# Optimization experiments

Hardware: AMD Instinct MI355X
Metric: run time of the kernel (lower is better)

## Reference

```python
import jax, jax.numpy as jnp
import numpy as np

H = 2048
V = 50257
M = 64

def setup_inputs() -> dict:
    key = jax.random.key(0)
    ks = jax.random.split(key, 14)
    s = 0.02  # weight init scale for numerical sanity
    return {
        "input_tok": jax.random.randint(ks[0], (1,), 0, V),
        "hidden": jax.random.normal(ks[1], (1, 1, H), jnp.float32),
        "encoder_outputs": jax.random.normal(ks[2], (M, H), jnp.float32),
        "emb": jax.random.normal(ks[3], (V, H), jnp.float32) * s,
        "attn_w": jax.random.normal(ks[4], (M, 2 * H), jnp.float32) * s,
        "attn_b": jax.random.normal(ks[5], (M,), jnp.float32) * s,
        "comb_w": jax.random.normal(ks[6], (H, 2 * H), jnp.float32) * s,
        "comb_b": jax.random.normal(ks[7], (H,), jnp.float32) * s,
        "w_ih": jax.random.normal(ks[8], (3 * H, H), jnp.float32) * s,
        "w_hh": jax.random.normal(ks[9], (3 * H, H), jnp.float32) * s,
        "b_ih": jax.random.normal(ks[10], (3 * H,), jnp.float32) * s,
        "b_hh": jax.random.normal(ks[11], (3 * H,), jnp.float32) * s,
        "out_w": jax.random.normal(ks[12], (V, H), jnp.float32) * s,
        "out_b": jax.random.normal(ks[13], (V,), jnp.float32) * s,
    }

def reference(input_tok, hidden, encoder_outputs, emb, attn_w, attn_b,
              comb_w, comb_b, w_ih, w_hh, b_ih, b_hh, out_w, out_b):
    # embedded: [1, H] (dropout is eval-mode identity)
    embedded = emb[input_tok].reshape(1, H)
    h0 = hidden[0]  # [1, H]
    # Bahdanau-style attention over encoder outputs
    attn_weights = jax.nn.softmax(
        jnp.concatenate([embedded, h0], axis=1) @ attn_w.T + attn_b, axis=1)  # [1, M]
    attn_applied = attn_weights @ encoder_outputs  # [1, H]
    # combine + relu
    x = jnp.concatenate([embedded, attn_applied], axis=1) @ comb_w.T + comb_b
    x = jax.nn.relu(x)  # [1, H] -> GRU input
    # single GRU cell step, PyTorch gate order (r, z, n)
    gi = x @ w_ih.T + b_ih   # [1, 3H]
    gh = h0 @ w_hh.T + b_hh  # [1, 3H]
    i_r, i_z, i_n = jnp.split(gi, 3, axis=1)
    h_r, h_z, h_n = jnp.split(gh, 3, axis=1)
    r = jax.nn.sigmoid(i_r + h_r)
    z = jax.nn.sigmoid(i_z + h_z)
    n = jnp.tanh(i_n + r * h_n)
    h_new = (1.0 - z) * n + z * h0  # [1, H]
    # output projection + log-softmax over vocab
    log_probs = jax.nn.log_softmax(h_new @ out_w.T + out_b, axis=1)  # [1, V]
    return (log_probs, h_new[None], attn_weights)
```

## Files before the change

kernel.cpp:

```cpp
#include <hip/hip_runtime.h>
#include <math.h>

#define H 2048
#define V 50257
#define M 64
#define NEG_BIG (-1.0e30f)

#define NB5 6283
#define NB6 197

typedef float f4 __attribute__((ext_vector_type(4)));

__device__ inline f4 ntload(const f4* p) { return __builtin_nontemporal_load(p); }
__device__ inline float dot4(f4 a, f4 b) { return a.x*b.x + a.y*b.y + a.z*b.z + a.w*b.w; }

__device__ inline float wred_sum(float v) {
#pragma unroll
    for (int o = 32; o >= 1; o >>= 1) v += __shfl_down(v, o);
    return v;
}

__global__ void k_scores_gh1(const int* __restrict__ tok, const float* __restrict__ hidden,
                             const float* __restrict__ emb, const float* __restrict__ attn_w,
                             const float* __restrict__ attn_b, const float* __restrict__ w_hh,
                             const float* __restrict__ b_hh, float* __restrict__ scores,
                             float* __restrict__ gh) {
    const int t = threadIdx.x, lane = t & 63, wid = t >> 6;
    if (blockIdx.x < 64) {
        const int m = blockIdx.x;
        const float* erow = emb + (size_t)tok[0] * H;
        const f4* w4 = (const f4*)(attn_w + (size_t)m * 2 * H);
        float acc = 0.f;
        for (int i = t; i < 1024; i += 256) {
            f4 w = ntload(w4 + i);
            int k = i * 4;
            f4 c = (k < H) ? *(const f4*)(erow + k) : *(const f4*)(hidden + (k - H));
            acc += dot4(w, c);
        }
        __shared__ float sred[4];
        float s = wred_sum(acc);
        if (lane == 0) sred[wid] = s;
        __syncthreads();
        if (t == 0) scores[m] = sred[0] + sred[1] + sred[2] + sred[3] + attn_b[m];
    } else {
        const int j = (blockIdx.x - 64) * 4 + wid;
        const f4* w4 = (const f4*)(w_hh + (size_t)j * H);
        const f4* h4 = (const f4*)hidden;
        float acc = 0.f;
#pragma unroll
        for (int it = 0; it < 8; ++it) {
            int i = it * 64 + lane;
            acc += dot4(ntload(w4 + i), h4[i]);
        }
        acc = wred_sum(acc);
        if (lane == 0) gh[j] = acc + b_hh[j];
    }
}

__global__ void k_sm_aa_gh2(const float* __restrict__ scores, const float* __restrict__ enc,
                            const float* __restrict__ hidden, const float* __restrict__ w_hh,
                            const float* __restrict__ b_hh, float* __restrict__ aw_out,
                            float* __restrict__ attn_applied, float* __restrict__ gh) {
    const int t = threadIdx.x, lane = t & 63, wid = t >> 6;
    if (blockIdx.x < 8) {
        __shared__ float w[M];
        if (t < 64) {
            float s = scores[t];
            float mx = s;
#pragma unroll
            for (int o = 32; o >= 1; o >>= 1) mx = fmaxf(mx, __shfl_xor(mx, o));
            float e = expf(s - mx);
            float sum = e;
#pragma unroll
            for (int o = 32; o >= 1; o >>= 1) sum += __shfl_xor(sum, o);
            float aw = e / sum;
            w[t] = aw;
            if (blockIdx.x == 0) aw_out[t] = aw;
        }
        __syncthreads();
        int h = blockIdx.x * 256 + t;
        float acc = 0.f;
#pragma unroll 8
        for (int m = 0; m < M; ++m) acc += w[m] * enc[(size_t)m * H + h];
        attn_applied[h] = acc;
    } else {
        const int j = 3072 + (blockIdx.x - 8) * 4 + wid;
        const f4* w4 = (const f4*)(w_hh + (size_t)j * H);
        const f4* h4 = (const f4*)hidden;
        float acc = 0.f;
#pragma unroll
        for (int it = 0; it < 8; ++it) {
            int i = it * 64 + lane;
            acc += dot4(ntload(w4 + i), h4[i]);
        }
        acc = wred_sum(acc);
        if (lane == 0) gh[j] = acc + b_hh[j];
    }
}

__global__ void k_combine(const int* __restrict__ tok, const float* __restrict__ emb,
                          const float* __restrict__ comb_w, const float* __restrict__ comb_b,
                          const float* __restrict__ aa, float* __restrict__ x_out) {
    int r = (blockIdx.x * blockDim.x + threadIdx.x) >> 6;
    int lane = threadIdx.x & 63;
    const float* erow = emb + (size_t)tok[0] * H;
    const f4* w4 = (const f4*)(comb_w + (size_t)r * 2 * H);
    float acc = 0.f;
#pragma unroll
    for (int it = 0; it < 16; ++it) {
        int i = it * 64 + lane;
        f4 w = ntload(w4 + i);
        int k = i * 4;
        f4 c = (k < H) ? *(const f4*)(erow + k) : *(const f4*)(aa + (k - H));
        acc += dot4(w, c);
    }
    acc = wred_sum(acc);
    if (lane == 0) x_out[r] = fmaxf(acc + comb_b[r], 0.f);
}

__global__ void k_gates(const float* __restrict__ hidden, const float* __restrict__ w_ih,
                        const float* __restrict__ b_ih, const float* __restrict__ x,
                        const float* __restrict__ gh, float* __restrict__ h_out) {
    int j = (blockIdx.x * blockDim.x + threadIdx.x) >> 6;
    int lane = threadIdx.x & 63;
    const f4* x4 = (const f4*)x;
    const f4* wr = (const f4*)(w_ih + (size_t)j * H);
    const f4* wz = (const f4*)(w_ih + (size_t)(H + j) * H);
    const f4* wn = (const f4*)(w_ih + (size_t)(2 * H + j) * H);
    float ar = 0.f, az = 0.f, an = 0.f;
#pragma unroll
    for (int it = 0; it < 8; ++it) {
        int i = it * 64 + lane;
        f4 xv = x4[i];
        ar += dot4(ntload(wr + i), xv);
        az += dot4(ntload(wz + i), xv);
        an += dot4(ntload(wn + i), xv);
    }
    ar = wred_sum(ar); az = wred_sum(az); an = wred_sum(an);
    if (lane == 0) {
        float r = 1.f / (1.f + expf(-(ar + b_ih[j] + gh[j])));
        float z = 1.f / (1.f + expf(-(az + b_ih[H + j] + gh[H + j])));
        float n = tanhf(an + b_ih[2 * H + j] + r * gh[2 * H + j]);
        h_out[j] = (1.f - z) * n + z * hidden[j];
    }
}

__global__ void k_logits(const float* __restrict__ out_w, const float* __restrict__ out_b,
                         const float* __restrict__ hnew, float* __restrict__ logits,
                         float2* __restrict__ part) {
    const int t = threadIdx.x, lane = t & 63, wid = t >> 6;
    const int base = (blockIdx.x * 4 + wid) * 2;
    const int row0 = base, row1 = base + 1;
    const bool v0 = row0 < V, v1 = row1 < V;
    const f4* w0 = (const f4*)(out_w + (size_t)(v0 ? row0 : 0) * H);
    const f4* w1 = (const f4*)(out_w + (size_t)(v1 ? row1 : 0) * H);
    const f4* h4 = (const f4*)hnew;
    float a0 = 0.f, a1 = 0.f;
#pragma unroll
    for (int it = 0; it < 8; ++it) {
        int i = it * 64 + lane;
        f4 h = h4[i];
        a0 += dot4(ntload(w0 + i), h);
        a1 += dot4(ntload(w1 + i), h);
    }
    a0 = wred_sum(a0); a1 = wred_sum(a1);
    float m = NEG_BIG, s = 0.f;
    if (lane == 0) {
        if (v0) { float lg = a0 + out_b[row0]; logits[row0] = lg; m = lg; s = 1.f; }
        if (v1) { float lg = a1 + out_b[row1]; logits[row1] = lg;
                  float mm = fmaxf(m, lg); s = s * expf(m - mm) + expf(lg - mm); m = mm; }
    }
    __shared__ float2 lms[4];
    if (lane == 0) lms[wid] = make_float2(m, s);
    __syncthreads();
    if (t == 0) {
        float gm = NEG_BIG, gs = 0.f;
#pragma unroll
        for (int i2 = 0; i2 < 4; ++i2) {
            float m2 = lms[i2].x, s2 = lms[i2].y;
            float mm = fmaxf(gm, m2);
            gs = gs * expf(gm - mm) + s2 * expf(m2 - mm);
            gm = mm;
        }
        part[blockIdx.x] = make_float2(gm, gs);
    }
}

__global__ void k_logsoftmax(float* __restrict__ logits, const float2* __restrict__ part) {
    const int t = threadIdx.x;
    float m = NEG_BIG, s = 0.f;
    for (int i = t; i < NB5; i += 256) {
        float2 p = part[i];
        float mm = fmaxf(m, p.x);
        s = s * expf(m - mm) + p.y * expf(p.x - mm);
        m = mm;
    }
    __shared__ float sm[256], ss[256];
    sm[t] = m; ss[t] = s;
    __syncthreads();
    for (int o = 128; o >= 1; o >>= 1) {
        if (t < o) {
            float m2 = sm[t + o], s2 = ss[t + o];
            float mm = fmaxf(sm[t], m2);
            ss[t] = ss[t] * expf(sm[t] - mm) + s2 * expf(m2 - mm);
            sm[t] = mm;
        }
        __syncthreads();
    }
    float lse = sm[0] + logf(ss[0]);
    int i = blockIdx.x * 256 + t;
    if (i < V) logits[i] -= lse;
}

extern "C" void kernel_launch(void* const* d_in, const int* in_sizes, int n_in,
                              void* d_out, int out_size, void* d_ws, size_t ws_size,
                              hipStream_t stream) {
    const int*   tok     = (const int*)d_in[0];
    const float* hidden  = (const float*)d_in[1];
    const float* enc     = (const float*)d_in[2];
    const float* emb     = (const float*)d_in[3];
    const float* attn_w  = (const float*)d_in[4];
    const float* attn_b  = (const float*)d_in[5];
    const float* comb_w  = (const float*)d_in[6];
    const float* comb_b  = (const float*)d_in[7];
    const float* w_ih    = (const float*)d_in[8];
    const float* w_hh    = (const float*)d_in[9];
    const float* b_ih    = (const float*)d_in[10];
    const float* b_hh    = (const float*)d_in[11];
    const float* out_w   = (const float*)d_in[12];
    const float* out_b   = (const float*)d_in[13];

    float* out = (float*)d_out;
    float* logp  = out;
    float* hout  = out + V;
    float* awout = out + V + H;

    float* ws = (float*)d_ws;
    float*  AA   = ws;
    float*  X    = ws + 2048;
    float*  SC   = ws + 4096;
    float*  GH   = ws + 4160;
    float2* PART = (float2*)(ws + 10304);

    k_scores_gh1<<<832, 256, 0, stream>>>(tok, hidden, emb, attn_w, attn_b, w_hh, b_hh, SC, GH);
    k_sm_aa_gh2 <<<776, 256, 0, stream>>>(SC, enc, hidden, w_hh, b_hh, awout, AA, GH);
    k_combine   <<<512, 256, 0, stream>>>(tok, emb, comb_w, comb_b, AA, X);
    k_gates     <<<512, 256, 0, stream>>>(hidden, w_ih, b_ih, X, GH, hout);
    k_logits    <<<NB5, 256, 0, stream>>>(out_w, out_b, hout, logp, PART);
    k_logsoftmax<<<NB6, 256, 0, stream>>>(logp, PART);
}
```

Measured before the change: 106.6 us.

## Hoist independent GRU hidden and combine-embedding matvecs into first kernel

```diff
diff --git a/kernel.cpp b/kernel.cpp
--- a/kernel.cpp
+++ b/kernel.cpp
@@ -20,14 +20,16 @@
     return v;
 }
 
-__global__ void k_scores_gh1(const int* __restrict__ tok, const float* __restrict__ hidden,
-                             const float* __restrict__ emb, const float* __restrict__ attn_w,
-                             const float* __restrict__ attn_b, const float* __restrict__ w_hh,
-                             const float* __restrict__ b_hh, float* __restrict__ scores,
-                             float* __restrict__ gh) {
+__global__ void k_indep(const int* __restrict__ tok, const float* __restrict__ hidden,
+                        const float* __restrict__ emb, const float* __restrict__ attn_w,
+                        const float* __restrict__ attn_b, const float* __restrict__ w_hh,
+                        const float* __restrict__ b_hh, const float* __restrict__ comb_w,
+                        float* __restrict__ scores, float* __restrict__ gh,
+                        float* __restrict__ pc) {
     const int t = threadIdx.x, lane = t & 63, wid = t >> 6;
-    if (blockIdx.x < 64) {
-        const int m = blockIdx.x;
+    const int b = blockIdx.x;
+    if (b < 64) {
+        const int m = b;
         const float* erow = emb + (size_t)tok[0] * H;
         const f4* w4 = (const f4*)(attn_w + (size_t)m * 2 * H);
         float acc = 0.f;
@@ -42,80 +44,77 @@
         if (lane == 0) sred[wid] = s;
         __syncthreads();
         if (t == 0) scores[m] = sred[0] + sred[1] + sred[2] + sred[3] + attn_b[m];
-    } else {
-        const int j = (blockIdx.x - 64) * 4 + wid;
-        const f4* w4 = (const f4*)(w_hh + (size_t)j * H);
+    } else if (b < 832) {
+        const int j0 = ((b - 64) * 4 + wid) * 2;
+        const f4* w0 = (const f4*)(w_hh + (size_t)j0 * H);
+        const f4* w1 = (const f4*)(w_hh + (size_t)(j0 + 1) * H);
         const f4* h4 = (const f4*)hidden;
-        float acc = 0.f;
+        float a0 = 0.f, a1 = 0.f;
 #pragma unroll
         for (int it = 0; it < 8; ++it) {
             int i = it * 64 + lane;
-            acc += dot4(ntload(w4 + i), h4[i]);
-        }
-        acc = wred_sum(acc);
-        if (lane == 0) gh[j] = acc + b_hh[j];
-    }
-}
-
-__global__ void k_sm_aa_gh2(const float* __restrict__ scores, const float* __restrict__ enc,
-                            const float* __restrict__ hidden, const float* __restrict__ w_hh,
-                            const float* __restrict__ b_hh, float* __restrict__ aw_out,
-                            float* __restrict__ attn_applied, float* __restrict__ gh) {
-    const int t = threadIdx.x, lane = t & 63, wid = t >> 6;
-    if (blockIdx.x < 8) {
-        __shared__ float w[M];
-        if (t < 64) {
-            float s = scores[t];
-            float mx = s;
-#pragma unroll
-            for (int o = 32; o >= 1; o >>= 1) mx = fmaxf(mx, __shfl_xor(mx, o));
-            float e = expf(s - mx);
-            float sum = e;
-#pragma unroll
-            for (int o = 32; o >= 1; o >>= 1) sum += __shfl_xor(sum, o);
-            float aw = e / sum;
-            w[t] = aw;
-            if (blockIdx.x == 0) aw_out[t] = aw;
-        }
-        __syncthreads();
-        int h = blockIdx.x * 256 + t;
-        float acc = 0.f;
-#pragma unroll 8
-        for (int m = 0; m < M; ++m) acc += w[m] * enc[(size_t)m * H + h];
-        attn_applied[h] = acc;
+            f4 hv = h4[i];
+            a0 += dot4(ntload(w0 + i), hv);
+            a1 += dot4(ntload(w1 + i), hv);
+        }
+        a0 = wred_sum(a0); a1 = wred_sum(a1);
+        if (lane == 0) { gh[j0] = a0 + b_hh[j0]; gh[j0 + 1] = a1 + b_hh[j0 + 1]; }
     } else {
-        const int j = 3072 + (blockIdx.x - 8) * 4 + wid;
-        const f4* w4 = (const f4*)(w_hh + (size_t)j * H);
-        const f4* h4 = (const f4*)hidden;
+        const int r = (b - 832) * 4 + wid;
+        const float* erow = emb + (size_t)tok[0] * H;
+        const f4* w4 = (const f4*)(comb_w + (size_t)r * 2 * H);
+        const f4* e4 = (const f4*)erow;
         float acc = 0.f;
 #pragma unroll
         for (int it = 0; it < 8; ++it) {
             int i = it * 64 + lane;
-            acc += dot4(ntload(w4 + i), h4[i]);
+            acc += dot4(ntload(w4 + i), e4[i]);
         }
         acc = wred_sum(acc);
-        if (lane == 0) gh[j] = acc + b_hh[j];
-    }
-}
-
-__global__ void k_combine(const int* __restrict__ tok, const float* __restrict__ emb,
-                          const float* __restrict__ comb_w, const float* __restrict__ comb_b,
-                          const float* __restrict__ aa, float* __restrict__ x_out) {
+        if (lane == 0) pc[r] = acc;
+    }
+}
+
+__global__ void k_sm_aa(const float* __restrict__ scores, const float* __restrict__ enc,
+                        float* __restrict__ aw_out, float* __restrict__ attn_applied) {
+    __shared__ float w[M];
+    int t = threadIdx.x;
+    if (t < 64) {
+        float s = scores[t];
+        float mx = s;
+#pragma unroll
+        for (int o = 32; o >= 1; o >>= 1) mx = fmaxf(mx, __shfl_xor(mx, o));
+        float e = expf(s - mx);
+        float sum = e;
+#pragma unroll
+        for (int o = 32; o >= 1; o >>= 1) sum += __shfl_xor(sum, o);
+        float aw = e / sum;
+        w[t] = aw;
+        if (blockIdx.x == 0) aw_out[t] = aw;
+    }
+    __syncthreads();
+    int h = blockIdx.x * 256 + t;
+    float acc = 0.f;
+#pragma unroll 8
+    for (int m = 0; m < M; ++m) acc += w[m] * enc[(size_t)m * H + h];
+    attn_applied[h] = acc;
+}
+
+__global__ void k_combine2(const float* __restrict__ comb_w, const float* __restrict__ comb_b,
+                           const float* __restrict__ aa, const float* __restrict__ pc,
+                           float* __restrict__ x_out) {
     int r = (blockIdx.x * blockDim.x + threadIdx.x) >> 6;
     int lane = threadIdx.x & 63;
-    const float* erow = emb + (size_t)tok[0] * H;
-    const f4* w4 = (const f4*)(comb_w + (size_t)r * 2 * H);
+    const f4* w4 = (const f4*)(comb_w + (size_t)r * 2 * H + H);
+    const f4* a4 = (const f4*)aa;
     float acc = 0.f;
 #pragma unroll
-    for (int it = 0; it < 16; ++it) {
+    for (int it = 0; it < 8; ++it) {
         int i = it * 64 + lane;
-        f4 w = ntload(w4 + i);
-        int k = i * 4;
-        f4 c = (k < H) ? *(const f4*)(erow + k) : *(const f4*)(aa + (k - H));
-        acc += dot4(w, c);
+        acc += dot4(ntload(w4 + i), a4[i]);
     }
     acc = wred_sum(acc);
-    if (lane == 0) x_out[r] = fmaxf(acc + comb_b[r], 0.f);
+    if (lane == 0) x_out[r] = fmaxf(pc[r] + acc + comb_b[r], 0.f);
 }
 
 __global__ void k_gates(const float* __restrict__ hidden, const float* __restrict__ w_ih,
@@ -240,12 +239,14 @@
     float*  X    = ws + 2048;
     float*  SC   = ws + 4096;
     float*  GH   = ws + 4160;
-    float2* PART = (float2*)(ws + 10304);
-
-    k_scores_gh1<<<832, 256, 0, stream>>>(tok, hidden, emb, attn_w, attn_b, w_hh, b_hh, SC, GH);
-    k_sm_aa_gh2 <<<776, 256, 0, stream>>>(SC, enc, hidden, w_hh, b_hh, awout, AA, GH);
-    k_combine   <<<512, 256, 0, stream>>>(tok, emb, comb_w, comb_b, AA, X);
-    k_gates     <<<512, 256, 0, stream>>>(hidden, w_ih, b_ih, X, GH, hout);
-    k_logits    <<<NB5, 256, 0, stream>>>(out_w, out_b, hout, logp, PART);
-    k_logsoftmax<<<NB6, 256, 0, stream>>>(logp, PART);
-}
+    float*  PC   = ws + 10304;
+    float2* PART = (float2*)(ws + 12352);
+
+    k_indep     <<<1344, 256, 0, stream>>>(tok, hidden, emb, attn_w, attn_b, w_hh, b_hh,
+                                           comb_w, SC, GH, PC);
+    k_sm_aa     <<<8,    256, 0, stream>>>(SC, enc, awout, AA);
+    k_combine2  <<<512,  256, 0, stream>>>(comb_w, comb_b, AA, PC, X);
+    k_gates     <<<512,  256, 0, stream>>>(hidden, w_ih, b_ih, X, GH, hout);
+    k_logits    <<<NB5,  256, 0, stream>>>(out_w, out_b, hout, logp, PART);
+    k_logsoftmax<<<NB6,  256, 0, stream>>>(logp, PART);
+}
```

New measurement: 107.1 us. No clear change (+0.5%).
